# Kernel optimization log

Hardware: AMD Instinct MI355X
Metric: run time of the kernel (lower is better)

## Reference

```python
import jax, jax.numpy as jnp
import numpy as np

DIST = 7
ROUNDS = 25
A = DIST ** 2 - 1              # n_ancillas = 48
ND = A * (A + 1) // 2          # 1176 upper-triangular entries


def _triangular_polmap():
    diag, nondiag = [], []
    for iy in range(A):
        for ix in range(iy, A):
            if ix != iy:
                nondiag.append(ix + iy * A)
            else:
                diag.append(ix + iy * A)
    return np.asarray(diag + nondiag, dtype=np.int32)

POLMAP = jnp.asarray(_triangular_polmap())  # (ND,)


def setup_inputs() -> dict:
    key = jax.random.key(0)
    k1, k2, k3 = jax.random.split(key, 3)
    x = jax.random.randint(k1, (4096, ROUNDS, A), 0, 2, dtype=jnp.int32)
    emb_diag = jax.random.normal(k2, (1, A), dtype=jnp.float32)
    emb_nondiag = jax.random.normal(k3, (1, ND - A, 4), dtype=jnp.float32)
    return {"x": x, "emb_diag": emb_diag, "emb_nondiag": emb_nondiag}


def reference(x, emb_diag, emb_nondiag):
    B, R, _ = x.shape
    # transformed embedding params (shared across rounds / batch via broadcast)
    sig_diag = jax.nn.sigmoid(emb_diag)                       # (1, A)
    f12 = jax.nn.sigmoid(emb_nondiag[:, :, 0])
    f9 = jax.nn.sigmoid(emb_nondiag[:, :, 1]) * f12
    f8 = jax.nn.sigmoid(emb_nondiag[:, :, 2]) * f9
    f6 = jax.nn.sigmoid(emb_nondiag[:, :, 3]) * f8
    fnd = jnp.stack([f12, f9, f8, f6], axis=2)                # (1, ND-A, 4)

    # sliding windows of 3 consecutive rounds, round axis leading for scan
    a = jnp.moveaxis(x[:, 0:R - 2, :], 1, 0)                  # (R-2, B, A)
    b = jnp.moveaxis(x[:, 1:R - 1, :], 1, 0)
    c = jnp.moveaxis(x[:, 2:R, :], 1, 0)

    def step(carry, abc):
        st, dt = carry                                         # int32 (B, A)
        ai, bi, ci = abc
        data_err = ai + ci - ai * ci * 2
        meas_err = bi * (1 - (ai + ci)) + ai * ci
        dt = dt * (1 - meas_err * 2)
        st = jnp.clip(st + dt * data_err, -1, 1)
        dt = dt * (1 - st * st * (1 - meas_err)) - st * (1 - meas_err)
        # quadratic (outer-product) state, values in {4,6,8,9,12,16}
        xx = st + 3
        outer = (xx[:, :, None] * xx[:, None, :]).reshape(B, A * A)
        tri = jnp.take(outer, POLMAP, axis=1)                  # (B, ND)
        rd, rn = tri[:, :A], tri[:, A:]
        diag_val = (rd == 16).astype(jnp.float32) + (rd == 9).astype(jnp.float32) * sig_diag
        nmask = jnp.stack([rn == 12, rn == 9, rn == 8, rn == 6], axis=2).astype(jnp.float32)
        nd_val = (rn == 16).astype(jnp.float32) + jnp.sum(nmask * fnd, axis=2)
        out = jnp.concatenate([diag_val, nd_val], axis=1)      # (B, ND)
        return (st, dt), out

    st0 = -jnp.ones((B, A), jnp.int32)
    dt0 = jnp.ones((B, A), jnp.int32)
    _, ys = jax.lax.scan(step, (st0, dt0), (a, b, c))          # (R-2, B, ND)
    return jnp.moveaxis(ys, 0, 1)                              # (B, R-2, ND)
```

## Files before the change

### kernel.cpp

```cpp
#include <hip/hip_runtime.h>
#include <math.h>

#define AA 48
#define RR 25
#define TT 23
#define ND 1176
#define NOFF 1128
#define BPB 4
#define NT 320
#define NOWN 294

#define GTAB_BYTES (ND * 16)

__global__ __launch_bounds__(256) void build_tables_kernel(
    const float* __restrict__ emb_diag,
    const float* __restrict__ emb_nd,
    float4* __restrict__ gtab,
    uint32_t* __restrict__ pairs)
{
    int p = blockIdx.x * 256 + threadIdx.x;
    if (p >= ND) return;
    if (p < AA) {
        pairs[p] = (uint32_t)(p | (p << 8));
        float s = 1.0f / (1.0f + __expf(-emb_diag[p]));
        gtab[p] = make_float4(0.0f, s, 0.0f, 0.0f);
    } else {
        int pp = p - AA;
        int iy = (int)((95.0f - sqrtf(9025.0f - 8.0f * (float)pp)) * 0.5f);
        if (iy < 0) iy = 0;
        if (iy > 46) iy = 46;
        while (iy < 46 && (47 * (iy + 1) - ((iy + 1) * iy) / 2) <= pp) ++iy;
        while (iy > 0 && (47 * iy - (iy * (iy - 1)) / 2) > pp) --iy;
        int S  = 47 * iy - (iy * (iy - 1)) / 2;
        int ix = iy + 1 + (pp - S);
        pairs[p] = (uint32_t)(iy | (ix << 8));
        const float* e = emb_nd + pp * 4;
        float f12 = 1.0f / (1.0f + __expf(-e[0]));
        float f9  = f12 / (1.0f + __expf(-e[1]));
        float f8  = f9  / (1.0f + __expf(-e[2]));
        float f6  = f8  / (1.0f + __expf(-e[3]));
        gtab[p] = make_float4(f12, f9, f8, f6);
    }
}

__global__ __launch_bounds__(NT) void cnn_embed_kernel(
    const int*      __restrict__ x,
    const float4*   __restrict__ gtab,
    const uint32_t* __restrict__ pairs,
    float*          __restrict__ out,
    int B)
{
    __shared__ uint8_t xls[BPB * RR * AA];
    __shared__ uint8_t xxc[BPB * TT * AA];

    const int tid = threadIdx.x;
    const int b0  = blockIdx.x * BPB;

    const bool owner = (tid < NOWN);
    int iidx[4], jidx[4];
    float4 g[4];
    if (owner) {
        uint4 pr = ((const uint4*)pairs)[tid];
        iidx[0] = pr.x & 0xFF; jidx[0] = (pr.x >> 8) & 0xFF;
        iidx[1] = pr.y & 0xFF; jidx[1] = (pr.y >> 8) & 0xFF;
        iidx[2] = pr.z & 0xFF; jidx[2] = (pr.z >> 8) & 0xFF;
        iidx[3] = pr.w & 0xFF; jidx[3] = (pr.w >> 8) & 0xFF;
        #pragma unroll
        for (int k = 0; k < 4; ++k) g[k] = gtab[4 * tid + k];
    }

    {
        int validB = B - b0;
        if (validB > BPB) validB = BPB;
        const int validInts = validB * RR * AA;
        const int4* xg = (const int4*)(x + (size_t)b0 * RR * AA);
        for (int gg = tid; gg * 4 < validInts; gg += NT) {
            int4 v = xg[gg];
            uint32_t packed = (uint32_t)(v.x & 1) | ((uint32_t)(v.y & 1) << 8) |
                              ((uint32_t)(v.z & 1) << 16) | ((uint32_t)(v.w & 1) << 24);
            *((uint32_t*)&xls[gg * 4]) = packed;
        }
    }
    __syncthreads();

    if (tid < BPB * AA) {
        const int bb = tid / AA;
        const int j  = tid - bb * AA;
        if (b0 + bb < B) {
            const uint8_t* xb  = &xls[bb * RR * AA];
            uint8_t*       xxb = &xxc[bb * TT * AA];
            int st = -1, dt = 1;
            #pragma unroll
            for (int t = 0; t < TT; ++t) {
                int a  = xb[t * AA + j];
                int bv = xb[(t + 1) * AA + j];
                int c  = xb[(t + 2) * AA + j];
                int de = a ^ c;
                int me = de ? 0 : (a ^ bv);
                if (me) dt = -dt;
                st += dt * de;
                st = st < -1 ? -1 : (st > 1 ? 1 : st);
                if (!me) dt = (st == 0) ? dt : -st;
                xxb[t * AA + j] = (uint8_t)(st + 3);
            }
        }
    }
    __syncthreads();

    if (owner) {
        #pragma unroll
        for (int bb = 0; bb < BPB; ++bb) {
            const int b = b0 + bb;
            if (b >= B) break;
            const uint8_t* xxb = &xxc[bb * TT * AA];
            float* ob = out + (size_t)b * TT * ND + tid * 4;
            for (int t = 0; t < TT; ++t) {
                const uint8_t* xr = &xxb[t * AA];
                float4 v;
                float* vf = (float*)&v;
                #pragma unroll
                for (int k = 0; k < 4; ++k) {
                    int prod = (int)xr[iidx[k]] * (int)xr[jidx[k]];
                    float r = 0.0f;
                    r = (prod == 6)  ? g[k].w : r;
                    r = (prod == 8)  ? g[k].z : r;
                    r = (prod == 9)  ? g[k].y : r;
                    r = (prod == 12) ? g[k].x : r;
                    r = (prod == 16) ? 1.0f   : r;
                    vf[k] = r;
                }
                *((float4*)(ob + t * ND)) = v;
            }
        }
    }
}

extern "C" void kernel_launch(void* const* d_in, const int* in_sizes, int n_in,
                              void* d_out, int out_size, void* d_ws, size_t ws_size,
                              hipStream_t stream) {
    const int*   x  = (const int*)d_in[0];
    const float* ed = (const float*)d_in[1];
    const float* en = (const float*)d_in[2];
    float* out = (float*)d_out;
    float4*   gtab  = (float4*)d_ws;
    uint32_t* pairs = (uint32_t*)((char*)d_ws + GTAB_BYTES);
    const int B = in_sizes[0] / (RR * AA);

    hipLaunchKernelGGL(build_tables_kernel, dim3((ND + 255) / 256), dim3(256), 0, stream,
                       ed, en, gtab, pairs);
    const int grid = (B + BPB - 1) / BPB;
    hipLaunchKernelGGL(cnn_embed_kernel, dim3(grid), dim3(NT), 0, stream,
                       x, gtab, pairs, out, B);
}
```

Measured before the change: 483.7 us.

## Replace compare-select chain with per-pair LDS lookup table indexed by state sum

```diff
diff --git a/kernel.cpp b/kernel.cpp
--- a/kernel.cpp
+++ b/kernel.cpp
@@ -5,25 +5,31 @@
 #define RR 25
 #define TT 23
 #define ND 1176
-#define NOFF 1128
 #define BPB 4
 #define NT 320
 #define NOWN 294
 
-#define GTAB_BYTES (ND * 16)
+#define LDS_XLS 0
+#define LDS_XXC 4800
+#define LDS_GT  9216
+#define LDS_TOT (LDS_GT + 4 * NOWN * 9 * 4)
+
+#define GT9_DWORDS (4 * NOWN * 9)
+#define GT9_BYTES  (GT9_DWORDS * 4)
 
 __global__ __launch_bounds__(256) void build_tables_kernel(
     const float* __restrict__ emb_diag,
     const float* __restrict__ emb_nd,
-    float4* __restrict__ gtab,
+    float*    __restrict__ gt9,
     uint32_t* __restrict__ pairs)
 {
     int p = blockIdx.x * 256 + threadIdx.x;
     if (p >= ND) return;
+    float v12 = 0.0f, v9 = 0.0f, v8 = 0.0f, v6 = 0.0f;
+    int i, j;
     if (p < AA) {
-        pairs[p] = (uint32_t)(p | (p << 8));
-        float s = 1.0f / (1.0f + __expf(-emb_diag[p]));
-        gtab[p] = make_float4(0.0f, s, 0.0f, 0.0f);
+        i = j = p;
+        v9 = 1.0f / (1.0f + __expf(-emb_diag[p]));
     } else {
         int pp = p - AA;
         int iy = (int)((95.0f - sqrtf(9025.0f - 8.0f * (float)pp)) * 0.5f);
@@ -31,42 +37,44 @@
         if (iy > 46) iy = 46;
         while (iy < 46 && (47 * (iy + 1) - ((iy + 1) * iy) / 2) <= pp) ++iy;
         while (iy > 0 && (47 * iy - (iy * (iy - 1)) / 2) > pp) --iy;
-        int S  = 47 * iy - (iy * (iy - 1)) / 2;
-        int ix = iy + 1 + (pp - S);
-        pairs[p] = (uint32_t)(iy | (ix << 8));
+        int S = 47 * iy - (iy * (iy - 1)) / 2;
+        i = iy; j = iy + 1 + (pp - S);
         const float* e = emb_nd + pp * 4;
-        float f12 = 1.0f / (1.0f + __expf(-e[0]));
-        float f9  = f12 / (1.0f + __expf(-e[1]));
-        float f8  = f9  / (1.0f + __expf(-e[2]));
-        float f6  = f8  / (1.0f + __expf(-e[3]));
-        gtab[p] = make_float4(f12, f9, f8, f6);
+        v12 = 1.0f / (1.0f + __expf(-e[0]));
+        v9  = v12 / (1.0f + __expf(-e[1]));
+        v8  = v9  / (1.0f + __expf(-e[2]));
+        v6  = v8  / (1.0f + __expf(-e[3]));
     }
+    pairs[p] = (uint32_t)(i | (j << 8));
+    int tid = p >> 2, k = p & 3;
+    float* row = gt9 + (k * NOWN + tid) * 9;
+    row[0] = 0.0f;
+    row[1] = 0.0f;
+    row[2] = v6;
+    row[3] = 0.0f;
+    row[4] = v8;
+    row[5] = v9;
+    row[6] = v12;
+    row[7] = 0.0f;
+    row[8] = 1.0f;
 }
 
 __global__ __launch_bounds__(NT) void cnn_embed_kernel(
     const int*      __restrict__ x,
-    const float4*   __restrict__ gtab,
+    const float*    __restrict__ gt9,
     const uint32_t* __restrict__ pairs,
     float*          __restrict__ out,
     int B)
 {
-    __shared__ uint8_t xls[BPB * RR * AA];
-    __shared__ uint8_t xxc[BPB * TT * AA];
+    __shared__ __align__(16) uint8_t smem[LDS_TOT];
 
     const int tid = threadIdx.x;
     const int b0  = blockIdx.x * BPB;
 
-    const bool owner = (tid < NOWN);
-    int iidx[4], jidx[4];
-    float4 g[4];
-    if (owner) {
-        uint4 pr = ((const uint4*)pairs)[tid];
-        iidx[0] = pr.x & 0xFF; jidx[0] = (pr.x >> 8) & 0xFF;
-        iidx[1] = pr.y & 0xFF; jidx[1] = (pr.y >> 8) & 0xFF;
-        iidx[2] = pr.z & 0xFF; jidx[2] = (pr.z >> 8) & 0xFF;
-        iidx[3] = pr.w & 0xFF; jidx[3] = (pr.w >> 8) & 0xFF;
-        #pragma unroll
-        for (int k = 0; k < 4; ++k) g[k] = gtab[4 * tid + k];
+    {
+        const float4* gsrc = (const float4*)gt9;
+        float4* gdst = (float4*)(smem + LDS_GT);
+        for (int g = tid; g < GT9_DWORDS / 4; g += NT) gdst[g] = gsrc[g];
     }
 
     {
@@ -78,7 +86,7 @@
             int4 v = xg[gg];
             uint32_t packed = (uint32_t)(v.x & 1) | ((uint32_t)(v.y & 1) << 8) |
                               ((uint32_t)(v.z & 1) << 16) | ((uint32_t)(v.w & 1) << 24);
-            *((uint32_t*)&xls[gg * 4]) = packed;
+            *((uint32_t*)&smem[LDS_XLS + gg * 4]) = packed;
         }
     }
     __syncthreads();
@@ -87,8 +95,8 @@
         const int bb = tid / AA;
         const int j  = tid - bb * AA;
         if (b0 + bb < B) {
-            const uint8_t* xb  = &xls[bb * RR * AA];
-            uint8_t*       xxb = &xxc[bb * TT * AA];
+            const uint8_t* xb  = smem + LDS_XLS + bb * RR * AA;
+            uint8_t*       xxb = smem + LDS_XXC + bb * TT * AA;
             int st = -1, dt = 1;
             #pragma unroll
             for (int t = 0; t < TT; ++t) {
@@ -107,27 +115,38 @@
     }
     __syncthreads();
 
-    if (owner) {
+    if (tid < NOWN) {
+        uint4 pr = ((const uint4*)pairs)[tid];
+        int ii[4], jj[4];
+        ii[0] = pr.x & 0xFF; jj[0] = (pr.x >> 8) & 0xFF;
+        ii[1] = pr.y & 0xFF; jj[1] = (pr.y >> 8) & 0xFF;
+        ii[2] = pr.z & 0xFF; jj[2] = (pr.z >> 8) & 0xFF;
+        ii[3] = pr.w & 0xFF; jj[3] = (pr.w >> 8) & 0xFF;
+        uint32_t rb[4];
+        #pragma unroll
+        for (int k = 0; k < 4; ++k)
+            rb[k] = (uint32_t)(LDS_GT + (k * NOWN + tid) * 36 - 32);
+
         #pragma unroll
         for (int bb = 0; bb < BPB; ++bb) {
             const int b = b0 + bb;
             if (b >= B) break;
-            const uint8_t* xxb = &xxc[bb * TT * AA];
+            const uint8_t* xr0 = smem + LDS_XXC + bb * TT * AA;
+            const uint8_t* pi[4], * pj[4];
+            #pragma unroll
+            for (int k = 0; k < 4; ++k) { pi[k] = xr0 + ii[k]; pj[k] = xr0 + jj[k]; }
             float* ob = out + (size_t)b * TT * ND + tid * 4;
+            #pragma unroll
             for (int t = 0; t < TT; ++t) {
-                const uint8_t* xr = &xxb[t * AA];
                 float4 v;
                 float* vf = (float*)&v;
                 #pragma unroll
                 for (int k = 0; k < 4; ++k) {
-                    int prod = (int)xr[iidx[k]] * (int)xr[jidx[k]];
-                    float r = 0.0f;
-                    r = (prod == 6)  ? g[k].w : r;
-                    r = (prod == 8)  ? g[k].z : r;
-                    r = (prod == 9)  ? g[k].y : r;
-                    r = (prod == 12) ? g[k].x : r;
-                    r = (prod == 16) ? 1.0f   : r;
-                    vf[k] = r;
+                    int ci = pi[k][t * AA];
+                    int cj = pj[k][t * AA];
+                    uint32_t off = rb[k] + (uint32_t)(ci + cj) * 8u +
+                                   (uint32_t)(ci & cj & 1) * 4u;
+                    vf[k] = *(const float*)&smem[off];
                 }
                 *((float4*)(ob + t * ND)) = v;
             }
@@ -142,13 +161,13 @@
     const float* ed = (const float*)d_in[1];
     const float* en = (const float*)d_in[2];
     float* out = (float*)d_out;
-    float4*   gtab  = (float4*)d_ws;
-    uint32_t* pairs = (uint32_t*)((char*)d_ws + GTAB_BYTES);
+    float*    gt9   = (float*)d_ws;
+    uint32_t* pairs = (uint32_t*)((char*)d_ws + GT9_BYTES);
     const int B = in_sizes[0] / (RR * AA);
 
     hipLaunchKernelGGL(build_tables_kernel, dim3((ND + 255) / 256), dim3(256), 0, stream,
-                       ed, en, gtab, pairs);
+                       ed, en, gt9, pairs);
     const int grid = (B + BPB - 1) / BPB;
     hipLaunchKernelGGL(cnn_embed_kernel, dim3(grid), dim3(NT), 0, stream,
-                       x, gtab, pairs, out, B);
+                       x, gt9, pairs, out, B);
 }
```

Result: no change. 487.7 us (+0.8%).
